# Kernel optimization log

Measured on AMD Instinct MI355X. Metric: run time of the kernel, lower is better.

Reference implementation:

```python
import jax, jax.numpy as jnp
import numpy as np

CHANNELS = 512
KSIZE = 5


def conv1d(x, w, b, pad):
    # x: (B, Cin, T), w: (Cout, Cin, k) -> (B, Cout, T)
    y = jax.lax.conv_general_dilated(
        x, w, window_strides=(1,), padding=[(pad, pad)],
        dimension_numbers=('NCH', 'OIH', 'NCH'))
    return y + b[None, :, None]


def setup_inputs() -> dict:
    key = jax.random.key(0)
    ks = jax.random.split(key, 10)
    B, C, T, K = 16, CHANNELS, 2048, KSIZE
    s = 0.02  # conv init scale
    return {
        'x': jax.random.normal(ks[0], (B, C, T), jnp.float32),
        'offset_w': jax.random.normal(ks[1], (2 * K, C, 3), jnp.float32) * s,
        'offset_b': jnp.zeros((2 * K,), jnp.float32),
        'mod_w': jax.random.normal(ks[2], (K, C, 3), jnp.float32) * s,
        'mod_b': jnp.zeros((K,), jnp.float32),
        'weight': jax.random.normal(ks[3], (C, C, K), jnp.float32),
        'rp1_w': jax.random.normal(ks[4], (C // 2, C, 3), jnp.float32) * s,
        'rp1_b': jnp.zeros((C // 2,), jnp.float32),
        'rp2_w': jax.random.normal(ks[5], (1, C // 2, 1), jnp.float32) * s,
        'rp2_b': jnp.zeros((1,), jnp.float32),
    }


def deformable_conv1d(x, offset, modulator, weight):
    B, C, T = x.shape
    K = weight.shape[-1]
    # offset: (B, 2K, T) -> (B, T, 2, K); only component 0 is used (as in torch src)
    off = offset.reshape(B, 2, K, T).transpose(0, 3, 1, 2)[:, :, 0, :]   # (B, T, K)
    mod = modulator.reshape(B, K, T).transpose(0, 2, 1)                   # (B, T, K)
    base = jnp.arange(T, dtype=x.dtype)[None, :, None]
    kpos = (jnp.arange(K, dtype=x.dtype) - K // 2)[None, None, :]
    pos = jnp.clip(base + kpos + off, 0, T - 1)                           # (B, T, K)
    pf = jnp.clip(jnp.floor(pos).astype(jnp.int32), 0, T - 1)
    pc = jnp.clip(jnp.ceil(pos).astype(jnp.int32), 0, T - 1)
    wf = pc.astype(x.dtype) - pos    # NB: both weights are 0 at integer pos (faithful to source)
    wc = pos - pf.astype(x.dtype)
    # gather along time for all channels at once: (B, C, T, K)
    sf = jnp.take_along_axis(x, pf.reshape(B, 1, T * K), axis=2).reshape(B, C, T, K)
    sc = jnp.take_along_axis(x, pc.reshape(B, 1, T * K), axis=2).reshape(B, C, T, K)
    sampled = sf * wf[:, None] + sc * wc[:, None]
    # only diagonal weight[c, c, k] is used in the source loops
    wdiag = weight[jnp.arange(C), jnp.arange(C), :]                       # (C, K)
    return jnp.einsum('bctk,ck,btk->bct', sampled, wdiag, mod)


def reference(x, offset_w, offset_b, mod_w, mod_b, weight, rp1_w, rp1_b, rp2_w, rp2_b):
    offset = conv1d(x, offset_w, offset_b, pad=1)            # (B, 2K, T)
    modulator = jax.nn.sigmoid(conv1d(x, mod_w, mod_b, pad=1))  # (B, K, T)
    deformed = deformable_conv1d(x, offset, modulator, weight)  # (B, C, T)
    h = jax.nn.relu(conv1d(deformed, rp1_w, rp1_b, pad=1))
    strength = conv1d(h, rp2_w, rp2_b, pad=0)[:, 0, :]          # (B, T)
    return deformed, strength
```

## Files before the change

kernel.cpp:

```cpp
#include <hip/hip_runtime.h>
#include <hip/hip_bf16.h>

#define CHN 512
#define TLEN 2048
#define KSZ 5
#define BATCH 16

typedef __hip_bfloat16 bf16;
typedef short bf16x8 __attribute__((ext_vector_type(8)));
typedef float f32x4  __attribute__((ext_vector_type(4)));

#define SAMP_BYTES (BATCH*TLEN*KSZ*8)
#define W1T_ELEMS  (16*4*3*64*40)
#define W1T_BYTES  (W1T_ELEMS*2)

__global__ __launch_bounds__(256) void kPrep(const float* __restrict__ w1,
    bf16* __restrict__ w1t, const float* __restrict__ ow,
    const float* __restrict__ mw, float* __restrict__ wpk,
    float* __restrict__ outs, const float* __restrict__ b2p)
{
  int bx = blockIdx.x;
  int tidl = threadIdx.x;
  if (bx < W1T_ELEMS/256) {
    int idx  = bx*256 + tidl;
    int c40  = idx % 40;
    int rest = idx / 40;
    int row  = rest & 63;
    int rr   = rest >> 6;
    int r    = rr % 3;
    int cq   = rr / 3;
    int q    = cq & 3;
    int ch   = cq >> 2;
    int co   = q*64 + row;
    float v = 0.f;
    if (c40 < 32) v = w1[(size_t)co*(CHN*3) + (ch*32 + c40)*3 + r];
    w1t[idx] = __float2bfloat16(v);
  } else if (bx < W1T_ELEMS/256 + 64) {
    int idx = (bx - W1T_ELEMS/256)*256 + tidl;
    int j = idx & 31, c = idx >> 5;
    float v = 0.f;
    if (j < 15)      { int o = j/3,  d = j - o*3;  v = ow[o*(CHN*3) + c*3 + d]; }
    else if (j < 30) { int jj = j-15; int o = jj/3, d = jj - o*3;
                       v = mw[o*(CHN*3) + c*3 + d]; }
    wpk[idx] = v;
  } else {
    outs[(bx - W1T_ELEMS/256 - 64)*256 + tidl] = b2p[0];
  }
}

__global__ __launch_bounds__(512) void kS(const float* __restrict__ x,
    const float* __restrict__ wpk, const float* __restrict__ ob,
    const float* __restrict__ mb, float2* __restrict__ samp)
{
  int b  = blockIdx.y;
  int t0 = blockIdx.x*64;
  int tx = threadIdx.x;
  int cg = threadIdx.y;
  int t  = t0 + tx;

  __shared__ float red[8][64][10];

  float acc[10];
  #pragma unroll
  for (int i=0;i<10;++i) acc[i]=0.f;
  const float* xb = x + (size_t)b*CHN*TLEN;
  int c0 = cg*64;
  #pragma unroll 4
  for (int c=c0;c<c0+64;++c) {
    int cu = __builtin_amdgcn_readfirstlane(c);
    const float* wp = wpk + cu*32;
    const float* xr = xb + (size_t)cu*TLEN;
    float xm = (t>0)      ? xr[t-1] : 0.f;
    float xc = xr[t];
    float xp = (t<TLEN-1) ? xr[t+1] : 0.f;
    #pragma unroll
    for (int o=0;o<5;++o) {
      acc[o]   = fmaf(xm, wp[o*3+0],    acc[o]);
      acc[o]   = fmaf(xc, wp[o*3+1],    acc[o]);
      acc[o]   = fmaf(xp, wp[o*3+2],    acc[o]);
      acc[5+o] = fmaf(xm, wp[15+o*3+0], acc[5+o]);
      acc[5+o] = fmaf(xc, wp[15+o*3+1], acc[5+o]);
      acc[5+o] = fmaf(xp, wp[15+o*3+2], acc[5+o]);
    }
  }
  #pragma unroll
  for (int i=0;i<10;++i) red[cg][tx][i] = acc[i];
  __syncthreads();
  for (int s=4;s>0;s>>=1) {
    if (cg < s) {
      #pragma unroll
      for (int i=0;i<10;++i) red[cg][tx][i] += red[cg+s][tx][i];
    }
    __syncthreads();
  }
  if (cg==0) {
    #pragma unroll
    for (int k=0;k<KSZ;++k) {
      float off = red[0][tx][k]   + ob[k];
      float mv  = red[0][tx][5+k] + mb[k];
      float sig = 1.f/(1.f + expf(-mv));
      float pos = (float)(t + k - 2) + off;
      pos = fminf(fmaxf(pos, 0.f), (float)(TLEN-1));
      samp[((size_t)b*TLEN + t)*KSZ + k] = make_float2(pos, sig);
    }
  }
}

#define BT   128
#define HALO 16
#define XLEN 160

__global__ __launch_bounds__(256) void kDf(const float* __restrict__ x,
    const float* __restrict__ wgt, const float2* __restrict__ sampg,
    float* __restrict__ out)
{
  int b  = blockIdx.z;
  int c0 = blockIdx.y*64;
  int t0 = blockIdx.x*BT;
  int tx = threadIdx.x, cy = threadIdx.y;
  int tid = cy*64 + tx;

  __shared__ float  xs[64*XLEN];
  __shared__ float2 sp[BT*KSZ];
  __shared__ int okf;

  int lo = min(max(t0 - HALO, 0), TLEN - XLEN);

  if (tid == 0) okf = 1;
  for (int i = tid; i < BT*KSZ; i += 256)
    sp[i] = sampg[((size_t)b*TLEN + t0)*KSZ + i];

  const float* xb = x + (size_t)b*CHN*TLEN;
  #pragma unroll
  for (int it = 0; it < 10; ++it) {
    int idx = tid + it*256;
    int c  = idx / 40;
    int c4 = idx - c*40;
    const float* src = xb + (size_t)(c0 + c)*TLEN + lo + c4*4;
    __builtin_amdgcn_global_load_lds(
        (const __attribute__((address_space(1))) unsigned int*)src,
        (__attribute__((address_space(3))) unsigned int*)&xs[idx*4],
        16, 0, 0);
  }
  __syncthreads();

  int   bl[2][KSZ];
  float wf[2][KSZ], wc[2][KSZ];
  bool ok = true;
  #pragma unroll
  for (int j=0;j<2;++j)
    #pragma unroll
    for (int k=0;k<KSZ;++k) {
      float2 s = sp[(j*64+tx)*KSZ + k];
      float pos = s.x, sig = s.y;
      float pf = floorf(pos), pc = ceilf(pos);
      int base = min((int)pf, TLEN-2);
      wf[j][k] = (pc - pos)*sig;
      wc[j][k] = (pos - pf)*sig;
      int bloc = base - lo;
      bl[j][k] = bloc;
      ok = ok && (bloc >= 0) && (bloc <= XLEN-2);
    }
  if (!ok) okf = 0;
  __syncthreads();
  int fast = okf;

  if (fast) {
    #pragma unroll 2
    for (int i=0;i<16;++i) {
      int cl = cy*16 + i;
      int cu = __builtin_amdgcn_readfirstlane(c0 + cl);
      const float* wd = wgt + (size_t)cu*(CHN*KSZ) + (size_t)cu*KSZ;
      float w0 = wd[0], w1v = wd[1], w2v = wd[2], w3 = wd[3], w4 = wd[4];
      const float* xr = xs + cl*XLEN;
      float o0, o1;
      {
        float a = 0.f;
        a = fmaf(fmaf(xr[bl[0][0]+1], wc[0][0], xr[bl[0][0]]*wf[0][0]), w0,  a);
        a = fmaf(fmaf(xr[bl[0][1]+1], wc[0][1], xr[bl[0][1]]*wf[0][1]), w1v, a);
        a = fmaf(fmaf(xr[bl[0][2]+1], wc[0][2], xr[bl[0][2]]*wf[0][2]), w2v, a);
        a = fmaf(fmaf(xr[bl[0][3]+1], wc[0][3], xr[bl[0][3]]*wf[0][3]), w3,  a);
        a = fmaf(fmaf(xr[bl[0][4]+1], wc[0][4], xr[bl[0][4]]*wf[0][4]), w4,  a);
        o0 = a;
      }
      {
        float a = 0.f;
        a = fmaf(fmaf(xr[bl[1][0]+1], wc[1][0], xr[bl[1][0]]*wf[1][0]), w0,  a);
        a = fmaf(fmaf(xr[bl[1][1]+1], wc[1][1], xr[bl[1][1]]*wf[1][1]), w1v, a);
        a = fmaf(fmaf(xr[bl[1][2]+1], wc[1][2], xr[bl[1][2]]*wf[1][2]), w2v, a);
        a = fmaf(fmaf(xr[bl[1][3]+1], wc[1][3], xr[bl[1][3]]*wf[1][3]), w3,  a);
        a = fmaf(fmaf(xr[bl[1][4]+1], wc[1][4], xr[bl[1][4]]*wf[1][4]), w4,  a);
        o1 = a;
      }
      size_t op = ((size_t)b*CHN + cu)*TLEN + t0 + tx;
      out[op]      = o0;
      out[op + 64] = o1;
    }
  } else {
    for (int i=0;i<16;++i) {
      int cl = cy*16 + i;
      int cu = __builtin_amdgcn_readfirstlane(c0 + cl);
      const float* wd = wgt + (size_t)cu*(CHN*KSZ) + (size_t)cu*KSZ;
      float wk0 = wd[0], wk1 = wd[1], wk2 = wd[2], wk3 = wd[3], wk4 = wd[4];
      const float* xr = xb + (size_t)cu*TLEN + lo;
      float o[2];
      #pragma unroll
      for (int j=0;j<2;++j) {
        float a = 0.f;
        a = fmaf(fmaf(xr[bl[j][0]+1], wc[j][0], xr[bl[j][0]]*wf[j][0]), wk0, a);
        a = fmaf(fmaf(xr[bl[j][1]+1], wc[j][1], xr[bl[j][1]]*wf[j][1]), wk1, a);
        a = fmaf(fmaf(xr[bl[j][2]+1], wc[j][2], xr[bl[j][2]]*wf[j][2]), wk2, a);
        a = fmaf(fmaf(xr[bl[j][3]+1], wc[j][3], xr[bl[j][3]]*wf[j][3]), wk3, a);
        a = fmaf(fmaf(xr[bl[j][4]+1], wc[j][4], xr[bl[j][4]]*wf[j][4]), wk4, a);
        o[j] = a;
      }
      size_t op = ((size_t)b*CHN + cu)*TLEN + t0 + tx;
      out[op]      = o[0];
      out[op + 64] = o[1];
    }
  }
}

#define DMA_WS(dst, ch_) do {                                                  \
  const char* gs = (const char*)(w1t + (size_t)((ch_)*4 + m0)*7680);           \
  char* ld = (char*)&Ws[dst][0];                                               \
  for (int of = tid*16; of < 15360; of += 4096) {                              \
    __builtin_amdgcn_global_load_lds(                                          \
        (const __attribute__((address_space(1))) unsigned int*)(gs + of),      \
        (__attribute__((address_space(3))) unsigned int*)(ld + of), 16, 0, 0); \
  }                                                                            \
} while(0)

#define LOAD_DT(ch_) do {                                                      \
  const float* dpb = def + ((size_t)b*CHN + (ch_)*32 + g*8)*TLEN;              \
  _Pragma("unroll")                                                            \
  for (int s=0;s<4;++s) {                                                      \
    int t = t0 - 1 + tl + s*64;                                                \
    _Pragma("unroll")                                                          \
    for (int j=0;j<8;++j)                                                      \
      rg[s][j] = (t>=0 && t<TLEN) ? dpb[(size_t)j*TLEN + t] : 0.f;             \
  }                                                                            \
  if (tl < 2) {                                                                \
    int t = t0 - 1 + 256 + tl;                                                 \
    _Pragma("unroll")                                                          \
    for (int j=0;j<8;++j)                                                      \
      rt[j] = (t<TLEN) ? dpb[(size_t)j*TLEN + t] : 0.f;                        \
  }                                                                            \
} while(0)

#define WRITE_DT(dst) do {                                                     \
  _Pragma("unroll")                                                            \
  for (int s=0;s<4;++s) {                                                      \
    bf16x8 v;                                                                  \
    _Pragma("unroll")                                                          \
    for (int j=0;j<8;++j) { union{bf16 h; short u;} cv;                        \
      cv.h = __float2bfloat16(rg[s][j]); v[j] = cv.u; }                        \
    *(bf16x8*)((char*)&Dt[dst][0] + (tl + s*64)*80 + g*16) = v;                \
  }                                                                            \
  if (tl < 2) {                                                                \
    bf16x8 v;                                                                  \
    _Pragma("unroll")                                                          \
    for (int j=0;j<8;++j) { union{bf16 h; short u;} cv;                        \
      cv.h = __float2bfloat16(rt[j]); v[j] = cv.u; }                           \
    *(bf16x8*)((char*)&Dt[dst][0] + (256 + tl)*80 + g*16) = v;                 \
  }                                                                            \
} while(0)

#define COMPUTE(cur) do {                                                      \
  _Pragma("unroll")                                                            \
  for (int r=0;r<3;++r) {                                                      \
    bf16x8 af[4], bfr[4];                                                      \
    _Pragma("unroll")                                                          \
    for (int mt=0;mt<4;++mt)                                                   \
      af[mt] = *(const bf16x8*)&Ws[cur][(size_t)(r*64 + mt*16 + ln15)*40 + quad*8];\
    _Pragma("unroll")                                                          \
    for (int nt=0;nt<4;++nt)                                                   \
      bfr[nt] = *(const bf16x8*)&Dt[cur][(size_t)(wN*64 + nt*16 + ln15 + r)*40 + quad*8];\
    _Pragma("unroll")                                                          \
    for (int mt=0;mt<4;++mt)                                                   \
      _Pragma("unroll")                                                        \
      for (int nt=0;nt<4;++nt)                                                 \
        acc[mt][nt] = __builtin_amdgcn_mfma_f32_16x16x32_bf16(                 \
            af[mt], bfr[nt], acc[mt][nt], 0, 0, 0);                            \
  }                                                                            \
} while(0)

__global__ __launch_bounds__(256, 2) void k2(const float* __restrict__ def,
    const bf16* __restrict__ w1t, const float* __restrict__ b1,
    const float* __restrict__ w2, float* __restrict__ outs)
{
  int n0 = blockIdx.x*256;
  int m0 = blockIdx.y;
  int b  = n0 / TLEN;
  int t0 = n0 % TLEN;
  int tid  = threadIdx.x;
  int lane = tid & 63;
  int wN   = tid >> 6;
  int ln15 = lane & 15, quad = lane >> 4;

  __shared__ bf16 Ws[2][3*64*40];
  __shared__ bf16 Dt[2][258*40];
  __shared__ float Ss[256];

  int g  = tid >> 6;
  int tl = tid & 63;

  f32x4 acc[4][4];
  #pragma unroll
  for (int i=0;i<4;++i)
    #pragma unroll
    for (int j=0;j<4;++j) acc[i][j] = (f32x4){0.f,0.f,0.f,0.f};

  float rg[4][8], rt[8];
  #pragma unroll
  for (int j=0;j<8;++j) rt[j] = 0.f;

  DMA_WS(0, 0);
  LOAD_DT(0);
  WRITE_DT(0);
  __syncthreads();

  for (int ch=0; ch<16; ++ch) {
    int cur = ch & 1;
    int nxt = cur ^ 1;
    if (ch < 15) {
      DMA_WS(nxt, ch+1);
      LOAD_DT(ch+1);
    }
    COMPUTE(cur);
    if (ch < 15)
      WRITE_DT(nxt);
    __syncthreads();
  }

  float part[4] = {0.f,0.f,0.f,0.f};
  #pragma unroll
  for (int mt=0;mt<4;++mt) {
    #pragma unroll
    for (int rr=0;rr<4;++rr) {
      int row = m0*64 + mt*16 + quad*4 + rr;
      float bias = b1[row];
      float wv   = w2[row];
      #pragma unroll
      for (int nt=0;nt<4;++nt) {
        float h = acc[mt][nt][rr] + bias;
        h = fmaxf(h, 0.f);
        part[nt] = fmaf(h, wv, part[nt]);
      }
    }
  }
  Ss[tid] = 0.f;
  __syncthreads();
  #pragma unroll
  for (int nt=0;nt<4;++nt)
    atomicAdd(&Ss[wN*64 + nt*16 + ln15], part[nt]);
  __syncthreads();
  atomicAdd(&outs[n0 + tid], Ss[tid]);
}

extern "C" void kernel_launch(void* const* d_in, const int* in_sizes, int n_in,
                              void* d_out, int out_size, void* d_ws, size_t ws_size,
                              hipStream_t stream) {
  const float* x  = (const float*)d_in[0];
  const float* ow = (const float*)d_in[1];
  const float* ob = (const float*)d_in[2];
  const float* mw = (const float*)d_in[3];
  const float* mb = (const float*)d_in[4];
  const float* wg = (const float*)d_in[5];
  const float* w1 = (const float*)d_in[6];
  const float* b1 = (const float*)d_in[7];
  const float* w2 = (const float*)d_in[8];
  const float* b2 = (const float*)d_in[9];

  float* out_def = (float*)d_out;
  float* out_str = out_def + (size_t)BATCH*CHN*TLEN;

  float2* samp = (float2*)d_ws;
  bf16*   w1t  = (bf16*)((char*)d_ws + SAMP_BYTES);
  float*  wpk  = (float*)((char*)d_ws + SAMP_BYTES + W1T_BYTES);

  kPrep<<<dim3(W1T_ELEMS/256 + 64 + 128), 256, 0, stream>>>(
      w1, w1t, ow, mw, wpk, out_str, b2);
  kS   <<<dim3(TLEN/64, BATCH), dim3(64,8), 0, stream>>>(x, wpk, ob, mb, samp);
  kDf  <<<dim3(TLEN/BT, CHN/64, BATCH), dim3(64,4), 0, stream>>>(x, wg, samp, out_def);
  k2   <<<dim3(BATCH*TLEN/256, 4), 256, 0, stream>>>(out_def, w1t, b1, w2, out_str);
}
```

Baseline: 229.0 us.

## Emit bf16 time-major deformed tensor from kDf and DMA it directly in k2

kDf now also writes a bf16 copy of the deformed output, packed into chunks of 32 channels laid out time-major with zero halo rows, into workspace. k2 can then load those tiles into LDS with global_load_lds DMA instead of reading fp32 through registers, converting to bf16 and writing LDS. This cuts k2's read traffic and VALU conversion work and lets the loads overlap with compute. The cost is an extra bf16 write from kDf and a larger workspace. A fallback to the old path is kept for when the workspace is too small.

```diff
diff --git a/kernel.cpp b/kernel.cpp
--- a/kernel.cpp
+++ b/kernel.cpp
@@ -13,15 +13,21 @@
 #define SAMP_BYTES (BATCH*TLEN*KSZ*8)
 #define W1T_ELEMS  (16*4*3*64*40)
 #define W1T_BYTES  (W1T_ELEMS*2)
+#define WPK_BYTES  65536
+#define DT_ROWS    2050
+#define DT_CHUNK   (DT_ROWS*32)
+#define DT_BYTES   ((size_t)BATCH*16*DT_CHUNK*2)
 
 __global__ __launch_bounds__(256) void kPrep(const float* __restrict__ w1,
     bf16* __restrict__ w1t, const float* __restrict__ ow,
     const float* __restrict__ mw, float* __restrict__ wpk,
-    float* __restrict__ outs, const float* __restrict__ b2p)
+    float* __restrict__ outs, const float* __restrict__ b2p,
+    bf16* __restrict__ dt)
 {
   int bx = blockIdx.x;
   int tidl = threadIdx.x;
-  if (bx < W1T_ELEMS/256) {
+  const int NP = W1T_ELEMS/256;
+  if (bx < NP) {
     int idx  = bx*256 + tidl;
     int c40  = idx % 40;
     int rest = idx / 40;
@@ -35,16 +41,22 @@
     float v = 0.f;
     if (c40 < 32) v = w1[(size_t)co*(CHN*3) + (ch*32 + c40)*3 + r];
     w1t[idx] = __float2bfloat16(v);
-  } else if (bx < W1T_ELEMS/256 + 64) {
-    int idx = (bx - W1T_ELEMS/256)*256 + tidl;
+  } else if (bx < NP + 64) {
+    int idx = (bx - NP)*256 + tidl;
     int j = idx & 31, c = idx >> 5;
     float v = 0.f;
     if (j < 15)      { int o = j/3,  d = j - o*3;  v = ow[o*(CHN*3) + c*3 + d]; }
     else if (j < 30) { int jj = j-15; int o = jj/3, d = jj - o*3;
                        v = mw[o*(CHN*3) + c*3 + d]; }
     wpk[idx] = v;
-  } else {
-    outs[(bx - W1T_ELEMS/256 - 64)*256 + tidl] = b2p[0];
+  } else if (bx < NP + 192) {
+    outs[(bx - NP - 64)*256 + tidl] = b2p[0];
+  } else if (dt) {
+    int z = (bx - NP - 192)*256 + tidl;
+    int chunk = z >> 6;
+    int row   = ((z >> 5) & 1) ? (DT_ROWS-1) : 0;
+    int col   = z & 31;
+    dt[(size_t)chunk*DT_CHUNK + row*32 + col] = __float2bfloat16(0.f);
   }
 }
 
@@ -110,9 +122,10 @@
 #define HALO 16
 #define XLEN 160
 
+template<bool WDT>
 __global__ __launch_bounds__(256) void kDf(const float* __restrict__ x,
     const float* __restrict__ wgt, const float2* __restrict__ sampg,
-    float* __restrict__ out)
+    float* __restrict__ out, bf16* __restrict__ dt)
 {
   int b  = blockIdx.z;
   int c0 = blockIdx.y*64;
@@ -165,8 +178,9 @@
   __syncthreads();
   int fast = okf;
 
+  unsigned pk0[8], pk1[8];
   if (fast) {
-    #pragma unroll 2
+    #pragma unroll
     for (int i=0;i<16;++i) {
       int cl = cy*16 + i;
       int cu = __builtin_amdgcn_readfirstlane(c0 + cl);
@@ -195,8 +209,17 @@
       size_t op = ((size_t)b*CHN + cu)*TLEN + t0 + tx;
       out[op]      = o0;
       out[op + 64] = o1;
+      if (WDT) {
+        union { bf16 h; unsigned short u; } cv0, cv1;
+        cv0.h = __float2bfloat16(o0);
+        cv1.h = __float2bfloat16(o1);
+        if (i & 1) { pk0[i>>1] |= (unsigned)cv0.u << 16;
+                     pk1[i>>1] |= (unsigned)cv1.u << 16; }
+        else       { pk0[i>>1]  = cv0.u;  pk1[i>>1]  = cv1.u; }
+      }
     }
   } else {
+    #pragma unroll
     for (int i=0;i<16;++i) {
       int cl = cy*16 + i;
       int cu = __builtin_amdgcn_readfirstlane(c0 + cl);
@@ -217,11 +240,31 @@
       size_t op = ((size_t)b*CHN + cu)*TLEN + t0 + tx;
       out[op]      = o[0];
       out[op + 64] = o[1];
-    }
+      if (WDT) {
+        union { bf16 h; unsigned short u; } cv0, cv1;
+        cv0.h = __float2bfloat16(o[0]);
+        cv1.h = __float2bfloat16(o[1]);
+        if (i & 1) { pk0[i>>1] |= (unsigned)cv0.u << 16;
+                     pk1[i>>1] |= (unsigned)cv1.u << 16; }
+        else       { pk0[i>>1]  = cv0.u;  pk1[i>>1]  = cv1.u; }
+      }
+    }
+  }
+
+  if (WDT) {
+    int ch   = (c0 >> 5) + (cy >> 1);
+    int colb = (cy & 1)*16;
+    bf16* p0 = dt + (size_t)(b*16 + ch)*DT_CHUNK
+                  + (size_t)(t0 + tx + 1)*32 + colb;
+    *(uint4*)p0       = make_uint4(pk0[0], pk0[1], pk0[2], pk0[3]);
+    *((uint4*)p0 + 1) = make_uint4(pk0[4], pk0[5], pk0[6], pk0[7]);
+    bf16* p1 = p0 + 64*32;
+    *(uint4*)p1       = make_uint4(pk1[0], pk1[1], pk1[2], pk1[3]);
+    *((uint4*)p1 + 1) = make_uint4(pk1[4], pk1[5], pk1[6], pk1[7]);
   }
 }
 
-#define DMA_WS(dst, ch_) do {                                                  \
+#define DMA_W2(dst, ch_) do {                                                  \
   const char* gs = (const char*)(w1t + (size_t)((ch_)*4 + m0)*7680);           \
   char* ld = (char*)&Ws[dst][0];                                               \
   for (int of = tid*16; of < 15360; of += 4096) {                              \
@@ -231,42 +274,18 @@
   }                                                                            \
 } while(0)
 
-#define LOAD_DT(ch_) do {                                                      \
-  const float* dpb = def + ((size_t)b*CHN + (ch_)*32 + g*8)*TLEN;              \
-  _Pragma("unroll")                                                            \
-  for (int s=0;s<4;++s) {                                                      \
-    int t = t0 - 1 + tl + s*64;                                                \
-    _Pragma("unroll")                                                          \
-    for (int j=0;j<8;++j)                                                      \
-      rg[s][j] = (t>=0 && t<TLEN) ? dpb[(size_t)j*TLEN + t] : 0.f;             \
-  }                                                                            \
-  if (tl < 2) {                                                                \
-    int t = t0 - 1 + 256 + tl;                                                 \
-    _Pragma("unroll")                                                          \
-    for (int j=0;j<8;++j)                                                      \
-      rt[j] = (t<TLEN) ? dpb[(size_t)j*TLEN + t] : 0.f;                        \
-  }                                                                            \
-} while(0)
-
-#define WRITE_DT(dst) do {                                                     \
-  _Pragma("unroll")                                                            \
-  for (int s=0;s<4;++s) {                                                      \
-    bf16x8 v;                                                                  \
-    _Pragma("unroll")                                                          \
-    for (int j=0;j<8;++j) { union{bf16 h; short u;} cv;                        \
-      cv.h = __float2bfloat16(rg[s][j]); v[j] = cv.u; }                        \
-    *(bf16x8*)((char*)&Dt[dst][0] + (tl + s*64)*80 + g*16) = v;                \
-  }                                                                            \
-  if (tl < 2) {                                                                \
-    bf16x8 v;                                                                  \
-    _Pragma("unroll")                                                          \
-    for (int j=0;j<8;++j) { union{bf16 h; short u;} cv;                        \
-      cv.h = __float2bfloat16(rt[j]); v[j] = cv.u; }                           \
-    *(bf16x8*)((char*)&Dt[dst][0] + (256 + tl)*80 + g*16) = v;                 \
-  }                                                                            \
-} while(0)
-
-#define COMPUTE(cur) do {                                                      \
+#define DMA_D2(dst, ch_) do {                                                  \
+  const char* gs = (const char*)(dt + (size_t)(b*16 + (ch_))*DT_CHUNK          \
+                                    + (size_t)t0*32);                          \
+  char* ld = (char*)&Dt[dst][0];                                               \
+  for (int of = tid*16; of < 16512; of += 4096) {                              \
+    __builtin_amdgcn_global_load_lds(                                          \
+        (const __attribute__((address_space(1))) unsigned int*)(gs + of),      \
+        (__attribute__((address_space(3))) unsigned int*)(ld + of), 16, 0, 0); \
+  }                                                                            \
+} while(0)
+
+#define COMPUTE2(cur) do {                                                     \
   _Pragma("unroll")                                                            \
   for (int r=0;r<3;++r) {                                                      \
     bf16x8 af[4], bfr[4];                                                      \
@@ -275,7 +294,7 @@
       af[mt] = *(const bf16x8*)&Ws[cur][(size_t)(r*64 + mt*16 + ln15)*40 + quad*8];\
     _Pragma("unroll")                                                          \
     for (int nt=0;nt<4;++nt)                                                   \
-      bfr[nt] = *(const bf16x8*)&Dt[cur][(size_t)(wN*64 + nt*16 + ln15 + r)*40 + quad*8];\
+      bfr[nt] = *(const bf16x8*)&Dt[cur][(size_t)(wN*64 + nt*16 + ln15 + r)*32 + quad*8];\
     _Pragma("unroll")                                                          \
     for (int mt=0;mt<4;++mt)                                                   \
       _Pragma("unroll")                                                        \
@@ -285,7 +304,7 @@
   }                                                                            \
 } while(0)
 
-__global__ __launch_bounds__(256, 2) void k2(const float* __restrict__ def,
+__global__ __launch_bounds__(256, 2) void k2d(const bf16* __restrict__ dt,
     const bf16* __restrict__ w1t, const float* __restrict__ b1,
     const float* __restrict__ w2, float* __restrict__ outs)
 {
@@ -299,37 +318,164 @@
   int ln15 = lane & 15, quad = lane >> 4;
 
   __shared__ bf16 Ws[2][3*64*40];
-  __shared__ bf16 Dt[2][258*40];
+  __shared__ bf16 Dt[2][258*32];
   __shared__ float Ss[256];
 
-  int g  = tid >> 6;
-  int tl = tid & 63;
-
   f32x4 acc[4][4];
   #pragma unroll
   for (int i=0;i<4;++i)
     #pragma unroll
     for (int j=0;j<4;++j) acc[i][j] = (f32x4){0.f,0.f,0.f,0.f};
 
-  float rg[4][8], rt[8];
-  #pragma unroll
-  for (int j=0;j<8;++j) rt[j] = 0.f;
-
-  DMA_WS(0, 0);
-  LOAD_DT(0);
-  WRITE_DT(0);
+  DMA_W2(0, 0);
+  DMA_D2(0, 0);
   __syncthreads();
 
   for (int ch=0; ch<16; ++ch) {
     int cur = ch & 1;
     int nxt = cur ^ 1;
     if (ch < 15) {
-      DMA_WS(nxt, ch+1);
-      LOAD_DT(ch+1);
-    }
-    COMPUTE(cur);
+      DMA_W2(nxt, ch+1);
+      DMA_D2(nxt, ch+1);
+    }
+    COMPUTE2(cur);
+    __syncthreads();
+  }
+
+  float part[4] = {0.f,0.f,0.f,0.f};
+  #pragma unroll
+  for (int mt=0;mt<4;++mt) {
+    #pragma unroll
+    for (int rr=0;rr<4;++rr) {
+      int row = m0*64 + mt*16 + quad*4 + rr;
+      float bias = b1[row];
+      float wv   = w2[row];
+      #pragma unroll
+      for (int nt=0;nt<4;++nt) {
+        float h = acc[mt][nt][rr] + bias;
+        h = fmaxf(h, 0.f);
+        part[nt] = fmaf(h, wv, part[nt]);
+      }
+    }
+  }
+  Ss[tid] = 0.f;
+  __syncthreads();
+  #pragma unroll
+  for (int nt=0;nt<4;++nt)
+    atomicAdd(&Ss[wN*64 + nt*16 + ln15], part[nt]);
+  __syncthreads();
+  atomicAdd(&outs[n0 + tid], Ss[tid]);
+}
+
+#define DMA_WSR(dst, ch_) do {                                                 \
+  const char* gs = (const char*)(w1t + (size_t)((ch_)*4 + m0)*7680);           \
+  char* ld = (char*)&Ws[dst][0];                                               \
+  for (int of = tid*16; of < 15360; of += 4096) {                              \
+    __builtin_amdgcn_global_load_lds(                                          \
+        (const __attribute__((address_space(1))) unsigned int*)(gs + of),      \
+        (__attribute__((address_space(3))) unsigned int*)(ld + of), 16, 0, 0); \
+  }                                                                            \
+} while(0)
+
+#define LOAD_DTR(ch_) do {                                                     \
+  const float* dpb = def + ((size_t)b*CHN + (ch_)*32 + g*8)*TLEN;              \
+  _Pragma("unroll")                                                            \
+  for (int s=0;s<4;++s) {                                                      \
+    int t = t0 - 1 + tl + s*64;                                                \
+    _Pragma("unroll")                                                          \
+    for (int j=0;j<8;++j)                                                      \
+      rg[s][j] = (t>=0 && t<TLEN) ? dpb[(size_t)j*TLEN + t] : 0.f;             \
+  }                                                                            \
+  if (tl < 2) {                                                                \
+    int t = t0 - 1 + 256 + tl;                                                 \
+    _Pragma("unroll")                                                          \
+    for (int j=0;j<8;++j)                                                      \
+      rt[j] = (t<TLEN) ? dpb[(size_t)j*TLEN + t] : 0.f;                        \
+  }                                                                            \
+} while(0)
+
+#define WRITE_DTR(dst) do {                                                    \
+  _Pragma("unroll")                                                            \
+  for (int s=0;s<4;++s) {                                                      \
+    bf16x8 v;                                                                  \
+    _Pragma("unroll")                                                          \
+    for (int j=0;j<8;++j) { union{bf16 h; short u;} cv;                        \
+      cv.h = __float2bfloat16(rg[s][j]); v[j] = cv.u; }                        \
+    *(bf16x8*)((char*)&Dt[dst][0] + (tl + s*64)*80 + g*16) = v;                \
+  }                                                                            \
+  if (tl < 2) {                                                                \
+    bf16x8 v;                                                                  \
+    _Pragma("unroll")                                                          \
+    for (int j=0;j<8;++j) { union{bf16 h; short u;} cv;                        \
+      cv.h = __float2bfloat16(rt[j]); v[j] = cv.u; }                           \
+    *(bf16x8*)((char*)&Dt[dst][0] + (256 + tl)*80 + g*16) = v;                 \
+  }                                                                            \
+} while(0)
+
+#define COMPUTER(cur) do {                                                     \
+  _Pragma("unroll")                                                            \
+  for (int r=0;r<3;++r) {                                                      \
+    bf16x8 af[4], bfr[4];                                                      \
+    _Pragma("unroll")                                                          \
+    for (int mt=0;mt<4;++mt)                                                   \
+      af[mt] = *(const bf16x8*)&Ws[cur][(size_t)(r*64 + mt*16 + ln15)*40 + quad*8];\
+    _Pragma("unroll")                                                          \
+    for (int nt=0;nt<4;++nt)                                                   \
+      bfr[nt] = *(const bf16x8*)&Dt[cur][(size_t)(wN*64 + nt*16 + ln15 + r)*40 + quad*8];\
+    _Pragma("unroll")                                                          \
+    for (int mt=0;mt<4;++mt)                                                   \
+      _Pragma("unroll")                                                        \
+      for (int nt=0;nt<4;++nt)                                                 \
+        acc[mt][nt] = __builtin_amdgcn_mfma_f32_16x16x32_bf16(                 \
+            af[mt], bfr[nt], acc[mt][nt], 0, 0, 0);                            \
+  }                                                                            \
+} while(0)
+
+__global__ __launch_bounds__(256, 2) void k2r(const float* __restrict__ def,
+    const bf16* __restrict__ w1t, const float* __restrict__ b1,
+    const float* __restrict__ w2, float* __restrict__ outs)
+{
+  int n0 = blockIdx.x*256;
+  int m0 = blockIdx.y;
+  int b  = n0 / TLEN;
+  int t0 = n0 % TLEN;
+  int tid  = threadIdx.x;
+  int lane = tid & 63;
+  int wN   = tid >> 6;
+  int ln15 = lane & 15, quad = lane >> 4;
+
+  __shared__ bf16 Ws[2][3*64*40];
+  __shared__ bf16 Dt[2][258*40];
+  __shared__ float Ss[256];
+
+  int g  = tid >> 6;
+  int tl = tid & 63;
+
+  f32x4 acc[4][4];
+  #pragma unroll
+  for (int i=0;i<4;++i)
+    #pragma unroll
+    for (int j=0;j<4;++j) acc[i][j] = (f32x4){0.f,0.f,0.f,0.f};
+
+  float rg[4][8], rt[8];
+  #pragma unroll
+  for (int j=0;j<8;++j) rt[j] = 0.f;
+
+  DMA_WSR(0, 0);
+  LOAD_DTR(0);
+  WRITE_DTR(0);
+  __syncthreads();
+
+  for (int ch=0; ch<16; ++ch) {
+    int cur = ch & 1;
+    int nxt = cur ^ 1;
+    if (ch < 15) {
+      DMA_WSR(nxt, ch+1);
+      LOAD_DTR(ch+1);
+    }
+    COMPUTER(cur);
     if (ch < 15)
-      WRITE_DT(nxt);
+      WRITE_DTR(nxt);
     __syncthreads();
   }
 
@@ -379,9 +525,21 @@
   bf16*   w1t  = (bf16*)((char*)d_ws + SAMP_BYTES);
   float*  wpk  = (float*)((char*)d_ws + SAMP_BYTES + W1T_BYTES);
 
-  kPrep<<<dim3(W1T_ELEMS/256 + 64 + 128), 256, 0, stream>>>(
-      w1, w1t, ow, mw, wpk, out_str, b2);
+  size_t need = (size_t)SAMP_BYTES + W1T_BYTES + WPK_BYTES + DT_BYTES;
+  bf16* dt = (ws_size >= need)
+      ? (bf16*)((char*)d_ws + SAMP_BYTES + W1T_BYTES + WPK_BYTES)
+      : nullptr;
+
+  kPrep<<<dim3(W1T_ELEMS/256 + 256), 256, 0, stream>>>(
+      w1, w1t, ow, mw, wpk, out_str, b2, dt);
   kS   <<<dim3(TLEN/64, BATCH), dim3(64,8), 0, stream>>>(x, wpk, ob, mb, samp);
-  kDf  <<<dim3(TLEN/BT, CHN/64, BATCH), dim3(64,4), 0, stream>>>(x, wg, samp, out_def);
-  k2   <<<dim3(BATCH*TLEN/256, 4), 256, 0, stream>>>(out_def, w1t, b1, w2, out_str);
+  if (dt) {
+    kDf<true> <<<dim3(TLEN/BT, CHN/64, BATCH), dim3(64,4), 0, stream>>>(
+        x, wg, samp, out_def, dt);
+    k2d<<<dim3(BATCH*TLEN/256, 4), 256, 0, stream>>>(dt, w1t, b1, w2, out_str);
+  } else {
+    kDf<false><<<dim3(TLEN/BT, CHN/64, BATCH), dim3(64,4), 0, stream>>>(
+        x, wg, samp, out_def, nullptr);
+    k2r<<<dim3(BATCH*TLEN/256, 4), 256, 0, stream>>>(out_def, w1t, b1, w2, out_str);
+  }
 }
```

Result: faster. 214.6 us (-6.3%).
